# Optimization experiments

Hardware: AMD Instinct MI355X
Metric: run time of the kernel (lower is better)

The kernel has to match this reference:

```python
import itertools
import jax, jax.numpy as jnp
import numpy as np

H, W, DIM, NH, WS = 64, 64, 384, 12, 7
HD = DIM // NH            # head dim = key_dim (attn_ratio=1)
N = WS * WS               # tokens per window
SCALE = HD ** -0.5
EPS = 1e-5
BATCH = 4
HID = int(DIM * 4.0)


def _bias_idxs():
    points = list(itertools.product(range(WS), range(WS)))
    offsets, idxs = {}, []
    for p1 in points:
        for p2 in points:
            off = (abs(p1[0] - p2[0]), abs(p1[1] - p2[1]))
            if off not in offsets:
                offsets[off] = len(offsets)
            idxs.append(offsets[off])
    return np.asarray(idxs, dtype=np.int32).reshape(N, N)

BIAS_IDXS = _bias_idxs()              # [N, N] static
NUM_OFFSETS = int(BIAS_IDXS.max()) + 1  # 49 for a 7x7 window


def setup_inputs() -> dict:
    key = jax.random.key(0)
    ks = jax.random.split(key, 10)
    rn = lambda k, shp, s=0.02: jax.random.normal(k, shp, jnp.float32) * s
    return {
        "x": jax.random.normal(ks[0], (BATCH, H * W, DIM), jnp.float32),
        "ln1_g": jnp.ones((DIM,), jnp.float32),
        "ln1_b": jnp.zeros((DIM,), jnp.float32),
        "qkv_w": rn(ks[1], (DIM, 3 * DIM)),
        "qkv_b": jnp.zeros((3 * DIM,), jnp.float32),
        "proj_w": rn(ks[2], (DIM, DIM)),
        "proj_b": jnp.zeros((DIM,), jnp.float32),
        "attn_bias": rn(ks[3], (NH, NUM_OFFSETS), 0.1),
        "conv_w": rn(ks[4], (DIM, 1, 3, 3), 0.1),  # depthwise OIHW
        "bn_g": jnp.ones((DIM,), jnp.float32),
        "bn_b": jnp.zeros((DIM,), jnp.float32),
        "bn_mean": rn(ks[5], (DIM,), 0.05),
        "bn_var": jax.random.uniform(ks[6], (DIM,), jnp.float32, 0.5, 1.5),
        "ln2_g": jnp.ones((DIM,), jnp.float32),
        "ln2_b": jnp.zeros((DIM,), jnp.float32),
        "fc1_w": rn(ks[7], (DIM, HID)),
        "fc1_b": jnp.zeros((HID,), jnp.float32),
        "fc2_w": rn(ks[8], (HID, DIM)),
        "fc2_b": jnp.zeros((DIM,), jnp.float32),
    }


def _ln(x, g, b):
    m = x.mean(-1, keepdims=True)
    v = jnp.var(x, axis=-1, keepdims=True)
    return (x - m) * jax.lax.rsqrt(v + EPS) * g + b


def reference(x, ln1_g, ln1_b, qkv_w, qkv_b, proj_w, proj_b, attn_bias,
              conv_w, bn_g, bn_b, bn_mean, bn_var, ln2_g, ln2_b,
              fc1_w, fc1_b, fc2_w, fc2_b):
    b, hw, c = x.shape
    res = x
    # --- window partition with padding ---
    pad_b = (-H) % WS
    pad_r = (-W) % WS
    pH, pW = H + pad_b, W + pad_r
    nH, nW = pH // WS, pW // WS
    xw = x.reshape(b, H, W, c)
    xw = jnp.pad(xw, ((0, 0), (0, pad_b), (0, pad_r), (0, 0)))
    xw = xw.reshape(b, nH, WS, nW, WS, c).transpose(0, 1, 3, 2, 4, 5)
    xw = xw.reshape(b * nH * nW, N, c)  # [Bw, N, C]
    # --- attention (pre-LN, relative position bias) ---
    xn = _ln(xw, ln1_g, ln1_b)
    qkv = (xn @ qkv_w + qkv_b).reshape(-1, N, NH, 3 * HD)
    q, k, v = jnp.split(qkv, [HD, 2 * HD], axis=-1)  # each [Bw, N, NH, HD]
    bias = attn_bias[:, BIAS_IDXS]                    # [NH, N, N]
    scores = jnp.einsum('bnhd,bmhd->bhnm', q, k) * SCALE + bias
    a = jax.nn.softmax(scores, axis=-1)
    o = jnp.einsum('bhnm,bmhd->bnhd', a, v).reshape(-1, N, NH * HD)
    xw = o @ proj_w + proj_b
    # --- window reverse + unpad ---
    xw = xw.reshape(b, nH, nW, WS, WS, c).transpose(0, 1, 3, 2, 4, 5)
    xw = xw.reshape(b, pH, pW, c)[:, :H, :W].reshape(b, hw, c)
    x = res + xw
    # --- depthwise 3x3 conv + BatchNorm (eval) ---
    xc = x.transpose(0, 2, 1).reshape(b, c, H, W)
    xc = jax.lax.conv_general_dilated(
        xc, conv_w, (1, 1), ((1, 1), (1, 1)),
        feature_group_count=c,
        dimension_numbers=('NCHW', 'OIHW', 'NCHW'))
    xc = (xc - bn_mean[:, None, None]) * jax.lax.rsqrt(bn_var[:, None, None] + EPS) \
         * bn_g[:, None, None] + bn_b[:, None, None]
    x = xc.reshape(b, c, hw).transpose(0, 2, 1)
    # --- MLP (pre-LN, GELU) with residual ---
    h1 = jax.nn.gelu(_ln(x, ln2_g, ln2_b) @ fc1_w + fc1_b, approximate=False)
    return x + (h1 @ fc2_w + fc2_b)
```

## Files before the change

### kernel.cpp

```cpp
#include <hip/hip_runtime.h>
#include <cstdint>


typedef __bf16 bf16x8 __attribute__((ext_vector_type(8)));
typedef __bf16 bf16x4 __attribute__((ext_vector_type(4)));
typedef float  f32x4  __attribute__((ext_vector_type(4)));

#define DIM_    384
#define QKVD    1152
#define HIDD    1536
#define NTOK    49
#define NWIN    400
#define TOKENS  16384
#define PADROW  16384
#define MQKV    16512
#define SCALE_  0.17677669529663689f
#define EPS_    1e-5f

#define B_LN1   8192
#define B_PADR  1
#define B_TQKV  108
#define B_TPROJ 36
#define B_TFC1  144
#define B_TFC2  144
#define B_CONV  14
#define B_BIAS  192
#define B_TOTAL (B_LN1 + B_PADR + B_TQKV + B_TPROJ + B_TFC1 + B_TFC2 + B_CONV + B_BIAS)

__device__ __forceinline__ void gload_lds16(const void* g, void* l) {
  __builtin_amdgcn_global_load_lds(
      (__attribute__((address_space(1))) void*)g,
      (__attribute__((address_space(3))) void*)l, 16, 0, 0);
}

__device__ __forceinline__ float gelu_fast(float v) {
  float t2 = v * (1.5957691216057308f + 0.07135481627f * v * v);
  return v * __builtin_amdgcn_rcpf(1.f + __expf(-t2));
}

__device__ __forceinline__ void tile_transpose(
    const float* __restrict__ src, __bf16* __restrict__ dst,
    int K, int N, int tile, int tilesN, __bf16 (*ld)[65]) {
  int kt = tile / tilesN, nt = tile % tilesN;
  int k0 = kt * 64, n0 = nt * 64;
  int tid = threadIdx.x;
  int a = tid & 63, b4 = tid >> 6;
  #pragma unroll
  for (int i = 0; i < 16; i++) {
    int kl = b4 + i * 4;
    ld[kl][a] = (__bf16)src[(long)(k0 + kl) * N + n0 + a];
  }
  __syncthreads();
  #pragma unroll
  for (int i = 0; i < 16; i++) {
    int nl = b4 + i * 4;
    dst[(long)(n0 + nl) * K + k0 + a] = ld[a][nl];
  }
}

__global__ __launch_bounds__(256) void prep_all(
    const float* __restrict__ x, const float* __restrict__ ln1_g,
    const float* __restrict__ ln1_b, __bf16* __restrict__ xn,
    const float* __restrict__ qkv_w,  __bf16* __restrict__ wqkv,
    const float* __restrict__ proj_w, __bf16* __restrict__ wproj,
    const float* __restrict__ fc1_w,  __bf16* __restrict__ wfc1,
    const float* __restrict__ fc2_w,  __bf16* __restrict__ wfc2,
    const float* __restrict__ conv_w, float* __restrict__ wconv,
    const float* __restrict__ attn_b, float* __restrict__ bm) {
  __shared__ __bf16 tlds[64][65];
  __shared__ float red[2][4];
  int b = blockIdx.x;
  int tid = threadIdx.x;

  if (b < B_LN1) {
    int sub = tid >> 7, tl = tid & 127;
    long t = (long)b * 2 + sub;
    const float* xr = x + t * DIM_;
    float v0 = xr[tl], v1 = xr[tl + 128], v2 = xr[tl + 256];
    float s = v0 + v1 + v2, s2 = v0 * v0 + v1 * v1 + v2 * v2;
    for (int off = 32; off; off >>= 1) { s += __shfl_down(s, off); s2 += __shfl_down(s2, off); }
    if ((tl & 63) == 0) { red[sub][tl >> 6] = s; red[sub][2 + (tl >> 6)] = s2; }
    __syncthreads();
    float S = red[sub][0] + red[sub][1], S2 = red[sub][2] + red[sub][3];
    float m  = S * (1.f / DIM_);
    float rs = rsqrtf(S2 * (1.f / DIM_) - m * m + EPS_);
    __bf16* orow = xn + t * DIM_;
    orow[tl]       = (__bf16)((v0 - m) * rs * ln1_g[tl]       + ln1_b[tl]);
    orow[tl + 128] = (__bf16)((v1 - m) * rs * ln1_g[tl + 128] + ln1_b[tl + 128]);
    orow[tl + 256] = (__bf16)((v2 - m) * rs * ln1_g[tl + 256] + ln1_b[tl + 256]);
    return;
  }
  b -= B_LN1;
  if (b < B_PADR) {
    for (int i = tid; i < DIM_; i += 256)
      xn[(long)PADROW * DIM_ + i] = (__bf16)ln1_b[i];
    return;
  }
  b -= B_PADR;
  if (b < B_TQKV)  { tile_transpose(qkv_w,  wqkv,  DIM_, QKVD, b, 18, tlds); return; }
  b -= B_TQKV;
  if (b < B_TPROJ) { tile_transpose(proj_w, wproj, DIM_, DIM_, b, 6,  tlds); return; }
  b -= B_TPROJ;
  if (b < B_TFC1)  { tile_transpose(fc1_w,  wfc1,  DIM_, HIDD, b, 24, tlds); return; }
  b -= B_TFC1;
  if (b < B_TFC2)  { tile_transpose(fc2_w,  wfc2,  HIDD, DIM_, b, 6,  tlds); return; }
  b -= B_TFC2;
  if (b < B_CONV) {
    int id = b * 256 + tid;
    if (id < 3456) {
      int ch = id / 9, k = id % 9;
      wconv[k * DIM_ + ch] = conv_w[id];
    }
    return;
  }
  b -= B_CONV;
  {
    int id = b * 256 + tid;
    int h = id >> 12, q = (id >> 6) & 63, kk = id & 63;
    float v;
    if (kk >= NTOK)      v = -1e30f;
    else if (q >= NTOK)  v = 0.f;
    else {
      int idx = abs(q / 7 - kk / 7) * 7 + abs(q % 7 - kk % 7);
      v = attn_b[h * NTOK + idx];
    }
    bm[id] = v;
  }
}

__global__ __launch_bounds__(384) void conv_bn_ln2(
    const float* __restrict__ x1, const float* __restrict__ wT,
    const float* __restrict__ bng, const float* __restrict__ bnb,
    const float* __restrict__ mean, const float* __restrict__ var,
    const float* __restrict__ g2, const float* __restrict__ b2,
    float* __restrict__ x2, __bf16* __restrict__ xln2) {
  int tid = threadIdx.x;
  int p = tid / 96, g = tid % 96;
  int pix = blockIdx.x * 4 + p;
  int bb = pix >> 12, rc = pix & 4095;
  int r = rc >> 6, c = rc & 63;
  int ch = g << 2;

  f32x4 acc = (f32x4){0.f, 0.f, 0.f, 0.f};
  #pragma unroll
  for (int dr = -1; dr <= 1; dr++) {
    int rr = r + dr;
    if (rr < 0 || rr >= 64) continue;
    #pragma unroll
    for (int dc = -1; dc <= 1; dc++) {
      int cc = c + dc;
      if (cc < 0 || cc >= 64) continue;
      f32x4 xv = *(const f32x4*)(x1 + ((long)bb * 4096 + rr * 64 + cc) * DIM_ + ch);
      f32x4 wv = *(const f32x4*)(wT + ((dr + 1) * 3 + (dc + 1)) * DIM_ + ch);
      acc += xv * wv;
    }
  }

  f32x4 gv = *(const f32x4*)(bng + ch);
  f32x4 vv = *(const f32x4*)(var + ch);
  f32x4 mv = *(const f32x4*)(mean + ch);
  f32x4 bv = *(const f32x4*)(bnb + ch);
  f32x4 y;
  #pragma unroll
  for (int j = 0; j < 4; j++) {
    float sc = gv[j] * rsqrtf(vv[j] + EPS_);
    y[j] = acc[j] * sc + (bv[j] - mv[j] * sc);
  }
  *(f32x4*)(x2 + (long)pix * DIM_ + ch) = y;

  __shared__ float pS[4][96], pS2[4][96], mS[4], rS[4];
  pS[p][g]  = y[0] + y[1] + y[2] + y[3];
  pS2[p][g] = y[0] * y[0] + y[1] * y[1] + y[2] * y[2] + y[3] * y[3];
  __syncthreads();
  if (g < 32) {
    float a  = pS[p][g]  + pS[p][g + 32]  + pS[p][g + 64];
    float a2 = pS2[p][g] + pS2[p][g + 32] + pS2[p][g + 64];
    #pragma unroll
    for (int off = 1; off < 32; off <<= 1) {
      a  += __shfl_xor(a, off);
      a2 += __shfl_xor(a2, off);
    }
    if (g == 0) {
      float m = a * (1.f / DIM_);
      mS[p] = m;
      rS[p] = rsqrtf(a2 * (1.f / DIM_) - m * m + EPS_);
    }
  }
  __syncthreads();
  float m = mS[p], rs = rS[p];
  f32x4 gg = *(const f32x4*)(g2 + ch);
  f32x4 b2v = *(const f32x4*)(b2 + ch);
  bf16x4 ov;
  #pragma unroll
  for (int j = 0; j < 4; j++) ov[j] = (__bf16)((y[j] - m) * rs * gg[j] + b2v[j]);
  *(bf16x4*)(xln2 + (long)pix * DIM_ + ch) = ov;
}

__global__ __launch_bounds__(64) void attn_mfma(const __bf16* __restrict__ qkv,
                                                const float* __restrict__ bm,
                                                __bf16* __restrict__ o) {
  int blk = blockIdx.x;
  int win = blk / 12, h = blk % 12;
  int bb = win / 100, rem = win % 100;
  int wy = rem / 10, wx = rem % 10;
  int lane = threadIdx.x;
  int quad = lane >> 4, l16 = lane & 15;

  __shared__ __align__(16) __bf16 Vt[32][72];
  __shared__ __align__(16) __bf16 P[64][72];

  const __bf16* base = qkv + h * 96;

  bf16x8 qf[4], kf[4];
  #pragma unroll
  for (int mt = 0; mt < 4; mt++) {
    int t = mt * 16 + l16;
    int ty = t / 7, tx = t % 7;
    int r = wy * 7 + ty, c = wx * 7 + tx;
    int row = (t < NTOK && r < 64 && c < 64) ? (bb * 4096 + r * 64 + c) : PADROW;
    const __bf16* rp = base + (long)row * QKVD + quad * 8;
    qf[mt] = *(const bf16x8*)(rp);
    kf[mt] = *(const bf16x8*)(rp + 32);
  }
  {
    int t = lane;
    int ty = t / 7, tx = t % 7;
    int r = wy * 7 + ty, c = wx * 7 + tx;
    int row = (t < NTOK && r < 64 && c < 64) ? (bb * 4096 + r * 64 + c) : PADROW;
    const __bf16* vp = base + (long)row * QKVD + 64;
    bf16x8 vv[4];
    #pragma unroll
    for (int i = 0; i < 4; i++) vv[i] = *(const bf16x8*)(vp + i * 8);
    #pragma unroll
    for (int i = 0; i < 4; i++)
      #pragma unroll
      for (int j = 0; j < 8; j++) Vt[i * 8 + j][lane] = vv[i][j];
  }

  f32x4 S[4][4];
  #pragma unroll
  for (int i = 0; i < 4; i++)
    #pragma unroll
    for (int j = 0; j < 4; j++) S[i][j] = (f32x4){0.f, 0.f, 0.f, 0.f};
  #pragma unroll
  for (int mt = 0; mt < 4; mt++)
    #pragma unroll
    for (int nt = 0; nt < 4; nt++)
      S[mt][nt] = __builtin_amdgcn_mfma_f32_16x16x32_bf16(qf[mt], kf[nt], S[mt][nt], 0, 0, 0);

  const float* bmh = bm + h * 4096;
  #pragma unroll
  for (int mt = 0; mt < 4; mt++)
    #pragma unroll
    for (int r = 0; r < 4; r++) {
      int q = mt * 16 + quad * 4 + r;
      #pragma unroll
      for (int nt = 0; nt < 4; nt++)
        S[mt][nt][r] = S[mt][nt][r] * SCALE_ + bmh[q * 64 + nt * 16 + l16];
    }

  #pragma unroll
  for (int mt = 0; mt < 4; mt++)
    #pragma unroll
    for (int r = 0; r < 4; r++) {
      float mx = fmaxf(fmaxf(S[mt][0][r], S[mt][1][r]), fmaxf(S[mt][2][r], S[mt][3][r]));
      #pragma unroll
      for (int off = 1; off < 16; off <<= 1) mx = fmaxf(mx, __shfl_xor(mx, off));
      float sum = 0.f;
      #pragma unroll
      for (int nt = 0; nt < 4; nt++) {
        float e = __expf(S[mt][nt][r] - mx);
        S[mt][nt][r] = e;
        sum += e;
      }
      #pragma unroll
      for (int off = 1; off < 16; off <<= 1) sum += __shfl_xor(sum, off);
      float inv = 1.f / sum;
      #pragma unroll
      for (int nt = 0; nt < 4; nt++) S[mt][nt][r] *= inv;
    }

  #pragma unroll
  for (int mt = 0; mt < 4; mt++)
    #pragma unroll
    for (int r = 0; r < 4; r++) {
      int q = mt * 16 + quad * 4 + r;
      #pragma unroll
      for (int nt = 0; nt < 4; nt++)
        P[q][nt * 16 + l16] = (__bf16)S[mt][nt][r];
    }
  __syncthreads();

  f32x4 O[4][2];
  #pragma unroll
  for (int i = 0; i < 4; i++)
    #pragma unroll
    for (int j = 0; j < 2; j++) O[i][j] = (f32x4){0.f, 0.f, 0.f, 0.f};
  #pragma unroll
  for (int kt = 0; kt < 2; kt++) {
    bf16x8 pf[4], vf[2];
    #pragma unroll
    for (int mt = 0; mt < 4; mt++)
      pf[mt] = *(const bf16x8*)(&P[mt * 16 + l16][kt * 32 + quad * 8]);
    #pragma unroll
    for (int nt = 0; nt < 2; nt++)
      vf[nt] = *(const bf16x8*)(&Vt[nt * 16 + l16][kt * 32 + quad * 8]);
    #pragma unroll
    for (int mt = 0; mt < 4; mt++)
      #pragma unroll
      for (int nt = 0; nt < 2; nt++)
        O[mt][nt] = __builtin_amdgcn_mfma_f32_16x16x32_bf16(pf[mt], vf[nt], O[mt][nt], 0, 0, 0);
  }

  #pragma unroll
  for (int mt = 0; mt < 4; mt++)
    #pragma unroll
    for (int r = 0; r < 4; r++) {
      int q = mt * 16 + quad * 4 + r;
      if (q < NTOK) {
        int ty = q / 7, tx = q % 7;
        int rr = wy * 7 + ty, cc = wx * 7 + tx;
        if (rr < 64 && cc < 64) {
          __bf16* ob = o + ((long)bb * 4096 + rr * 64 + cc) * DIM_ + h * 32;
          #pragma unroll
          for (int nt = 0; nt < 2; nt++)
            ob[nt * 16 + l16] = (__bf16)O[mt][nt][r];
        }
      }
    }
}

template <int MODE, int TN>
__global__ void __launch_bounds__(256)
gemm_bf16(const __bf16* __restrict__ A, const __bf16* __restrict__ Bt,
          const float* __restrict__ bias, int K, int N,
          float* __restrict__ outf, __bf16* __restrict__ outb,
          const float* __restrict__ res) {
  constexpr int NT = TN / 32;
  __shared__ __align__(16) __bf16 sA[128 * 32];
  int tid = threadIdx.x, lane = tid & 63, wid = tid >> 6;
  int wm = wid >> 1, wn = wid & 1;
  int quad = lane >> 4, l16 = lane & 15;
  long tileM = (long)blockIdx.x * 128;
  long tileN = (long)blockIdx.y * TN;

  f32x4 acc[4][NT];
  #pragma unroll
  for (int i = 0; i < 4; i++)
    #pragma unroll
    for (int j = 0; j < NT; j++) acc[i][j] = (f32x4){0.f, 0.f, 0.f, 0.f};

  int rr = wid * 16 + (lane >> 2);
  const __bf16* gA = A + (tileM + rr) * (long)K + ((lane & 3) << 3);
  const long rowskip = 64 * (long)K;
  const __bf16* bP[NT];
  #pragma unroll
  for (int nt = 0; nt < NT; nt++)
    bP[nt] = Bt + (tileN + wn * (TN / 2) + nt * 16 + l16) * (long)K + (quad << 3);

  for (int k0 = 0; k0 < K; k0 += 32) {
    gload_lds16(gA + k0,           sA + (wid << 9));
    gload_lds16(gA + k0 + rowskip, sA + ((wid + 4) << 9));
    bf16x8 bfr[NT];
    #pragma unroll
    for (int nt = 0; nt < NT; nt++) bfr[nt] = *(const bf16x8*)(bP[nt] + k0);
    __syncthreads();
    bf16x8 af[4];
    #pragma unroll
    for (int mt = 0; mt < 4; mt++)
      af[mt] = *(const bf16x8*)(sA + ((wm * 64 + mt * 16 + l16) << 5) + (quad << 3));
    #pragma unroll
    for (int mt = 0; mt < 4; mt++)
      #pragma unroll
      for (int nt = 0; nt < NT; nt++)
        acc[mt][nt] = __builtin_amdgcn_mfma_f32_16x16x32_bf16(af[mt], bfr[nt], acc[mt][nt], 0, 0, 0);
    __syncthreads();
  }

  float bcol[NT];
  #pragma unroll
  for (int nt = 0; nt < NT; nt++) bcol[nt] = bias[tileN + wn * (TN / 2) + nt * 16 + l16];

  #pragma unroll
  for (int mt = 0; mt < 4; mt++) {
    #pragma unroll
    for (int r = 0; r < 4; r++) {
      long row = tileM + wm * 64 + mt * 16 + quad * 4 + r;
      if (MODE == 0) {
        __bf16* orow = outb + row * (long)N;
        #pragma unroll
        for (int nt = 0; nt < NT; nt++)
          orow[tileN + wn * (TN / 2) + nt * 16 + l16] = (__bf16)(acc[mt][nt][r] + bcol[nt]);
      } else if (MODE == 2) {
        __bf16* orow = outb + row * (long)N;
        #pragma unroll
        for (int nt = 0; nt < NT; nt++) {
          float v = acc[mt][nt][r] + bcol[nt];
          orow[tileN + wn * (TN / 2) + nt * 16 + l16] = (__bf16)gelu_fast(v);
        }
      } else {
        float* orow = outf + row * (long)N;
        const float* rrow = res + row * (long)N;
        #pragma unroll
        for (int nt = 0; nt < NT; nt++) {
          long col = tileN + wn * (TN / 2) + nt * 16 + l16;
          orow[col] = acc[mt][nt][r] + bcol[nt] + rrow[col];
        }
      }
    }
  }
}

extern "C" void kernel_launch(void* const* d_in, const int* in_sizes, int n_in,
                              void* d_out, int out_size, void* d_ws, size_t ws_size,
                              hipStream_t stream) {
  const float* x       = (const float*)d_in[0];
  const float* ln1_g   = (const float*)d_in[1];
  const float* ln1_b   = (const float*)d_in[2];
  const float* qkv_w   = (const float*)d_in[3];
  const float* qkv_b   = (const float*)d_in[4];
  const float* proj_w  = (const float*)d_in[5];
  const float* proj_b  = (const float*)d_in[6];
  const float* attn_b  = (const float*)d_in[7];
  const float* conv_w  = (const float*)d_in[8];
  const float* bn_g    = (const float*)d_in[9];
  const float* bn_b    = (const float*)d_in[10];
  const float* bn_mean = (const float*)d_in[11];
  const float* bn_var  = (const float*)d_in[12];
  const float* ln2_g   = (const float*)d_in[13];
  const float* ln2_b   = (const float*)d_in[14];
  const float* fc1_w   = (const float*)d_in[15];
  const float* fc1_b   = (const float*)d_in[16];
  const float* fc2_w   = (const float*)d_in[17];
  const float* fc2_b   = (const float*)d_in[18];

  char* p = (char*)d_ws;
  __bf16* WQKV = (__bf16*)p;  p += 884736;
  __bf16* WPROJ = (__bf16*)p; p += 294912;
  __bf16* WFC1 = (__bf16*)p;  p += 1179648;
  __bf16* WFC2 = (__bf16*)p;  p += 1179648;
  float*  WCONV = (float*)p;  p += 13824;
  char* region = p;           p += 63307776;
  float* X1 = (float*)p;      p += 25165824;
  float* X2 = (float*)p;      p += 25165824;
  __bf16* XN   = (__bf16*)region;
  __bf16* QKVB = (__bf16*)(region + 12681216);
  __bf16* OBUF = (__bf16*)(region + 50724864);
  __bf16* XLN2 = (__bf16*)region;
  __bf16* H1   = (__bf16*)(region + 12681216);
  float*  BM   = X1;
  float* OUT = (float*)d_out;

  prep_all<<<B_TOTAL, 256, 0, stream>>>(x, ln1_g, ln1_b, XN,
                                        qkv_w, WQKV, proj_w, WPROJ,
                                        fc1_w, WFC1, fc2_w, WFC2,
                                        conv_w, WCONV, attn_b, BM);

  gemm_bf16<0, 128><<<dim3(MQKV / 128, QKVD / 128), 256, 0, stream>>>(
      XN, WQKV, qkv_b, DIM_, QKVD, nullptr, QKVB, nullptr);

  attn_mfma<<<NWIN * 12, 64, 0, stream>>>(QKVB, BM, OBUF);

  gemm_bf16<3, 64><<<dim3(TOKENS / 128, DIM_ / 64), 256, 0, stream>>>(
      OBUF, WPROJ, proj_b, DIM_, DIM_, X1, nullptr, x);

  conv_bn_ln2<<<TOKENS / 4, 384, 0, stream>>>(X1, WCONV, bn_g, bn_b, bn_mean, bn_var,
                                              ln2_g, ln2_b, X2, XLN2);

  gemm_bf16<2, 128><<<dim3(TOKENS / 128, HIDD / 128), 256, 0, stream>>>(
      XLN2, WFC1, fc1_b, DIM_, HIDD, nullptr, H1, nullptr);

  gemm_bf16<3, 64><<<dim3(TOKENS / 128, DIM_ / 64), 256, 0, stream>>>(
      H1, WFC2, fc2_b, HIDD, DIM_, OUT, nullptr, X2);
}
```

Baseline: 322.5 us.

## Stage GEMM B tiles through LDS and add K=64 FC2 kernel

The generic bf16 GEMM now loads the weight (B) tile into shared memory with direct global-to-LDS loads, instead of each wave reading B fragments straight from global memory. A new FC2-specific kernel handles the K=1536 GEMM by loading two 32-wide K slices per iteration, which halves the number of barriers per K step. The aim is to cut redundant global traffic for B and the synchronisation overhead, at the cost of more LDS per block.

New measurement: 278.6 us. 1.16x faster.

```diff
diff --git a/kernel.cpp b/kernel.cpp
--- a/kernel.cpp
+++ b/kernel.cpp
@@ -338,6 +338,7 @@
           const float* __restrict__ res) {
   constexpr int NT = TN / 32;
   __shared__ __align__(16) __bf16 sA[128 * 32];
+  __shared__ __align__(16) __bf16 sB[TN * 32];
   int tid = threadIdx.x, lane = tid & 63, wid = tid >> 6;
   int wm = wid >> 1, wn = wid & 1;
   int quad = lane >> 4, l16 = lane & 15;
@@ -351,24 +352,24 @@
     for (int j = 0; j < NT; j++) acc[i][j] = (f32x4){0.f, 0.f, 0.f, 0.f};
 
   int rr = wid * 16 + (lane >> 2);
-  const __bf16* gA = A + (tileM + rr) * (long)K + ((lane & 3) << 3);
+  const __bf16* gA = A  + (tileM + rr) * (long)K + ((lane & 3) << 3);
+  const __bf16* gB = Bt + (tileN + rr) * (long)K + ((lane & 3) << 3);
   const long rowskip = 64 * (long)K;
-  const __bf16* bP[NT];
-  #pragma unroll
-  for (int nt = 0; nt < NT; nt++)
-    bP[nt] = Bt + (tileN + wn * (TN / 2) + nt * 16 + l16) * (long)K + (quad << 3);
 
   for (int k0 = 0; k0 < K; k0 += 32) {
     gload_lds16(gA + k0,           sA + (wid << 9));
     gload_lds16(gA + k0 + rowskip, sA + ((wid + 4) << 9));
-    bf16x8 bfr[NT];
-    #pragma unroll
-    for (int nt = 0; nt < NT; nt++) bfr[nt] = *(const bf16x8*)(bP[nt] + k0);
+    gload_lds16(gB + k0,           sB + (wid << 9));
+    if (TN == 128)
+      gload_lds16(gB + k0 + rowskip, sB + ((wid + 4) << 9));
     __syncthreads();
-    bf16x8 af[4];
+    bf16x8 af[4], bfr[NT];
     #pragma unroll
     for (int mt = 0; mt < 4; mt++)
       af[mt] = *(const bf16x8*)(sA + ((wm * 64 + mt * 16 + l16) << 5) + (quad << 3));
+    #pragma unroll
+    for (int nt = 0; nt < NT; nt++)
+      bfr[nt] = *(const bf16x8*)(sB + ((wn * (TN / 2) + nt * 16 + l16) << 5) + (quad << 3));
     #pragma unroll
     for (int mt = 0; mt < 4; mt++)
       #pragma unroll
@@ -411,6 +412,77 @@
   }
 }
 
+__global__ void __launch_bounds__(256)
+gemm_fc2_k64(const __bf16* __restrict__ A, const __bf16* __restrict__ Bt,
+             const float* __restrict__ bias, int K, int N,
+             float* __restrict__ outf, const float* __restrict__ res) {
+  constexpr int TN = 64, NT = 2;
+  __shared__ __align__(16) __bf16 sA[2][128 * 32];
+  __shared__ __align__(16) __bf16 sB[2][TN * 32];
+  int tid = threadIdx.x, lane = tid & 63, wid = tid >> 6;
+  int wm = wid >> 1, wn = wid & 1;
+  int quad = lane >> 4, l16 = lane & 15;
+  long tileM = (long)blockIdx.x * 128;
+  long tileN = (long)blockIdx.y * TN;
+
+  f32x4 acc[4][NT];
+  #pragma unroll
+  for (int i = 0; i < 4; i++)
+    #pragma unroll
+    for (int j = 0; j < NT; j++) acc[i][j] = (f32x4){0.f, 0.f, 0.f, 0.f};
+
+  int rr = wid * 16 + (lane >> 2);
+  const __bf16* gA = A  + (tileM + rr) * (long)K + ((lane & 3) << 3);
+  const __bf16* gB = Bt + (tileN + rr) * (long)K + ((lane & 3) << 3);
+  const long rowskip = 64 * (long)K;
+
+  for (int k0 = 0; k0 < K; k0 += 64) {
+    #pragma unroll
+    for (int h = 0; h < 2; h++) {
+      const int ko = k0 + h * 32;
+      gload_lds16(gA + ko,           &sA[h][wid << 9]);
+      gload_lds16(gA + ko + rowskip, &sA[h][(wid + 4) << 9]);
+      gload_lds16(gB + ko,           &sB[h][wid << 9]);
+    }
+    __syncthreads();
+    #pragma unroll
+    for (int h = 0; h < 2; h++) {
+      bf16x8 af[4], bfr[NT];
+      #pragma unroll
+      for (int mt = 0; mt < 4; mt++)
+        af[mt] = *(const bf16x8*)(&sA[h][((wm * 64 + mt * 16 + l16) << 5) + (quad << 3)]);
+      #pragma unroll
+      for (int nt = 0; nt < NT; nt++)
+        bfr[nt] = *(const bf16x8*)(&sB[h][((wn * 32 + nt * 16 + l16) << 5) + (quad << 3)]);
+      #pragma unroll
+      for (int mt = 0; mt < 4; mt++)
+        #pragma unroll
+        for (int nt = 0; nt < NT; nt++)
+          acc[mt][nt] = __builtin_amdgcn_mfma_f32_16x16x32_bf16(af[mt], bfr[nt], acc[mt][nt], 0, 0, 0);
+    }
+    __syncthreads();
+  }
+
+  float bcol[NT];
+  #pragma unroll
+  for (int nt = 0; nt < NT; nt++) bcol[nt] = bias[tileN + wn * 32 + nt * 16 + l16];
+
+  #pragma unroll
+  for (int mt = 0; mt < 4; mt++) {
+    #pragma unroll
+    for (int r = 0; r < 4; r++) {
+      long row = tileM + wm * 64 + mt * 16 + quad * 4 + r;
+      float* orow = outf + row * (long)N;
+      const float* rrow = res + row * (long)N;
+      #pragma unroll
+      for (int nt = 0; nt < NT; nt++) {
+        long col = tileN + wn * 32 + nt * 16 + l16;
+        orow[col] = acc[mt][nt][r] + bcol[nt] + rrow[col];
+      }
+    }
+  }
+}
+
 extern "C" void kernel_launch(void* const* d_in, const int* in_sizes, int n_in,
                               void* d_out, int out_size, void* d_ws, size_t ws_size,
                               hipStream_t stream) {
@@ -470,6 +542,6 @@
   gemm_bf16<2, 128><<<dim3(TOKENS / 128, HIDD / 128), 256, 0, stream>>>(
       XLN2, WFC1, fc1_b, DIM_, HIDD, nullptr, H1, nullptr);
 
-  gemm_bf16<3, 64><<<dim3(TOKENS / 128, DIM_ / 64), 256, 0, stream>>>(
-      H1, WFC2, fc2_b, HIDD, DIM_, OUT, nullptr, X2);
-}
+  gemm_fc2_k64<<<dim3(TOKENS / 128, DIM_ / 64), 256, 0, stream>>>(
+      H1, WFC2, fc2_b, HIDD, DIM_, OUT, X2);
+}
```

## Stage B tiles in LDS with K=64 steps and store intermediates as bf16

Applied to the files above, without the earlier changes.

Replaces the GEMM with a variant that stages both the A and B tiles into LDS using swizzled slots. Each barrier pair now covers two 32-wide K halves, and all GEMMs use a fixed 64-wide N tile. The intermediate residual buffers X1 and X2 are stored as bf16 instead of fp32, and the attention bias mask gets its own buffer. The aim is to cut global memory traffic and barrier count, and to drop uncoalesced direct B loads from global memory. The risk is precision loss on the residual path and more blocks for the QKV and FC1 GEMMs, which reload the A tiles more often.

New measurement: 283.9 us. 1.14x faster.

```diff
diff --git a/kernel.cpp b/kernel.cpp
--- a/kernel.cpp
+++ b/kernel.cpp
@@ -129,11 +129,11 @@
 }
 
 __global__ __launch_bounds__(384) void conv_bn_ln2(
-    const float* __restrict__ x1, const float* __restrict__ wT,
+    const __bf16* __restrict__ x1, const float* __restrict__ wT,
     const float* __restrict__ bng, const float* __restrict__ bnb,
     const float* __restrict__ mean, const float* __restrict__ var,
     const float* __restrict__ g2, const float* __restrict__ b2,
-    float* __restrict__ x2, __bf16* __restrict__ xln2) {
+    __bf16* __restrict__ x2, __bf16* __restrict__ xln2) {
   int tid = threadIdx.x;
   int p = tid / 96, g = tid % 96;
   int pix = blockIdx.x * 4 + p;
@@ -150,9 +150,10 @@
     for (int dc = -1; dc <= 1; dc++) {
       int cc = c + dc;
       if (cc < 0 || cc >= 64) continue;
-      f32x4 xv = *(const f32x4*)(x1 + ((long)bb * 4096 + rr * 64 + cc) * DIM_ + ch);
+      bf16x4 xb = *(const bf16x4*)(x1 + ((long)bb * 4096 + rr * 64 + cc) * DIM_ + ch);
       f32x4 wv = *(const f32x4*)(wT + ((dr + 1) * 3 + (dc + 1)) * DIM_ + ch);
-      acc += xv * wv;
+      #pragma unroll
+      for (int j = 0; j < 4; j++) acc[j] += (float)xb[j] * wv[j];
     }
   }
 
@@ -166,7 +167,12 @@
     float sc = gv[j] * rsqrtf(vv[j] + EPS_);
     y[j] = acc[j] * sc + (bv[j] - mv[j] * sc);
   }
-  *(f32x4*)(x2 + (long)pix * DIM_ + ch) = y;
+  {
+    bf16x4 xv2;
+    #pragma unroll
+    for (int j = 0; j < 4; j++) xv2[j] = (__bf16)y[j];
+    *(bf16x4*)(x2 + (long)pix * DIM_ + ch) = xv2;
+  }
 
   __shared__ float pS[4][96], pS2[4][96], mS[4], rS[4];
   pS[p][g]  = y[0] + y[1] + y[2] + y[3];
@@ -330,14 +336,15 @@
     }
 }
 
-template <int MODE, int TN>
+template <int MODE>
 __global__ void __launch_bounds__(256)
-gemm_bf16(const __bf16* __restrict__ A, const __bf16* __restrict__ Bt,
-          const float* __restrict__ bias, int K, int N,
-          float* __restrict__ outf, __bf16* __restrict__ outb,
-          const float* __restrict__ res) {
-  constexpr int NT = TN / 32;
-  __shared__ __align__(16) __bf16 sA[128 * 32];
+gemm_k64(const __bf16* __restrict__ A, const __bf16* __restrict__ Bt,
+         const float* __restrict__ bias, int K, int N,
+         float* __restrict__ outf, __bf16* __restrict__ outb,
+         const void* __restrict__ res) {
+  constexpr int TN = 64, NT = 2;
+  __shared__ __align__(16) __bf16 sA[2][128 * 32];
+  __shared__ __align__(16) __bf16 sB[2][TN * 32];
   int tid = threadIdx.x, lane = tid & 63, wid = tid >> 6;
   int wm = wid >> 1, wn = wid & 1;
   int quad = lane >> 4, l16 = lane & 15;
@@ -351,35 +358,42 @@
     for (int j = 0; j < NT; j++) acc[i][j] = (f32x4){0.f, 0.f, 0.f, 0.f};
 
   int rr = wid * 16 + (lane >> 2);
-  const __bf16* gA = A + (tileM + rr) * (long)K + ((lane & 3) << 3);
+  int sc = ((lane & 3) - (lane >> 3)) & 3;
+  const __bf16* gA = A  + (tileM + rr) * (long)K + (sc << 3);
+  const __bf16* gB = Bt + (tileN + rr) * (long)K + (sc << 3);
   const long rowskip = 64 * (long)K;
-  const __bf16* bP[NT];
-  #pragma unroll
-  for (int nt = 0; nt < NT; nt++)
-    bP[nt] = Bt + (tileN + wn * (TN / 2) + nt * 16 + l16) * (long)K + (quad << 3);
-
-  for (int k0 = 0; k0 < K; k0 += 32) {
-    gload_lds16(gA + k0,           sA + (wid << 9));
-    gload_lds16(gA + k0 + rowskip, sA + ((wid + 4) << 9));
-    bf16x8 bfr[NT];
-    #pragma unroll
-    for (int nt = 0; nt < NT; nt++) bfr[nt] = *(const bf16x8*)(bP[nt] + k0);
+  int slot = (((l16 >> 1) + quad) & 3) << 3;
+
+  for (int k0 = 0; k0 < K; k0 += 64) {
+    #pragma unroll
+    for (int h = 0; h < 2; h++) {
+      const int ko = k0 + h * 32;
+      gload_lds16(gA + ko,           &sA[h][wid << 9]);
+      gload_lds16(gA + ko + rowskip, &sA[h][(wid + 4) << 9]);
+      gload_lds16(gB + ko,           &sB[h][wid << 9]);
+    }
     __syncthreads();
-    bf16x8 af[4];
-    #pragma unroll
-    for (int mt = 0; mt < 4; mt++)
-      af[mt] = *(const bf16x8*)(sA + ((wm * 64 + mt * 16 + l16) << 5) + (quad << 3));
-    #pragma unroll
-    for (int mt = 0; mt < 4; mt++)
+    #pragma unroll
+    for (int h = 0; h < 2; h++) {
+      bf16x8 af[4], bfr[NT];
+      #pragma unroll
+      for (int mt = 0; mt < 4; mt++)
+        af[mt] = *(const bf16x8*)(&sA[h][((wm * 64 + mt * 16 + l16) << 5) + slot]);
       #pragma unroll
       for (int nt = 0; nt < NT; nt++)
-        acc[mt][nt] = __builtin_amdgcn_mfma_f32_16x16x32_bf16(af[mt], bfr[nt], acc[mt][nt], 0, 0, 0);
+        bfr[nt] = *(const bf16x8*)(&sB[h][((wn * 32 + nt * 16 + l16) << 5) + slot]);
+      #pragma unroll
+      for (int mt = 0; mt < 4; mt++)
+        #pragma unroll
+        for (int nt = 0; nt < NT; nt++)
+          acc[mt][nt] = __builtin_amdgcn_mfma_f32_16x16x32_bf16(af[mt], bfr[nt], acc[mt][nt], 0, 0, 0);
+    }
     __syncthreads();
   }
 
   float bcol[NT];
   #pragma unroll
-  for (int nt = 0; nt < NT; nt++) bcol[nt] = bias[tileN + wn * (TN / 2) + nt * 16 + l16];
+  for (int nt = 0; nt < NT; nt++) bcol[nt] = bias[tileN + wn * 32 + nt * 16 + l16];
 
   #pragma unroll
   for (int mt = 0; mt < 4; mt++) {
@@ -390,21 +404,29 @@
         __bf16* orow = outb + row * (long)N;
         #pragma unroll
         for (int nt = 0; nt < NT; nt++)
-          orow[tileN + wn * (TN / 2) + nt * 16 + l16] = (__bf16)(acc[mt][nt][r] + bcol[nt]);
+          orow[tileN + wn * 32 + nt * 16 + l16] = (__bf16)(acc[mt][nt][r] + bcol[nt]);
       } else if (MODE == 2) {
         __bf16* orow = outb + row * (long)N;
         #pragma unroll
         for (int nt = 0; nt < NT; nt++) {
           float v = acc[mt][nt][r] + bcol[nt];
-          orow[tileN + wn * (TN / 2) + nt * 16 + l16] = (__bf16)gelu_fast(v);
+          orow[tileN + wn * 32 + nt * 16 + l16] = (__bf16)gelu_fast(v);
+        }
+      } else if (MODE == 4) {
+        float* orow = outf + row * (long)N;
+        const __bf16* rrow = (const __bf16*)res + row * (long)N;
+        #pragma unroll
+        for (int nt = 0; nt < NT; nt++) {
+          long col = tileN + wn * 32 + nt * 16 + l16;
+          orow[col] = acc[mt][nt][r] + bcol[nt] + (float)rrow[col];
         }
       } else {
-        float* orow = outf + row * (long)N;
-        const float* rrow = res + row * (long)N;
+        __bf16* orow = outb + row * (long)N;
+        const float* rrow = (const float*)res + row * (long)N;
         #pragma unroll
         for (int nt = 0; nt < NT; nt++) {
-          long col = tileN + wn * (TN / 2) + nt * 16 + l16;
-          orow[col] = acc[mt][nt][r] + bcol[nt] + rrow[col];
+          long col = tileN + wn * 32 + nt * 16 + l16;
+          orow[col] = (__bf16)(acc[mt][nt][r] + bcol[nt] + rrow[col]);
         }
       }
     }
@@ -441,14 +463,15 @@
   __bf16* WFC2 = (__bf16*)p;  p += 1179648;
   float*  WCONV = (float*)p;  p += 13824;
   char* region = p;           p += 63307776;
-  float* X1 = (float*)p;      p += 25165824;
-  float* X2 = (float*)p;      p += 25165824;
+  float* BMbuf = (float*)p;   p += 196608;
+  __bf16* X1 = (__bf16*)p;    p += 12582912;
+  __bf16* X2 = (__bf16*)p;    p += 12582912;
   __bf16* XN   = (__bf16*)region;
   __bf16* QKVB = (__bf16*)(region + 12681216);
   __bf16* OBUF = (__bf16*)(region + 50724864);
   __bf16* XLN2 = (__bf16*)region;
   __bf16* H1   = (__bf16*)(region + 12681216);
-  float*  BM   = X1;
+  float*  BM   = BMbuf;
   float* OUT = (float*)d_out;
 
   prep_all<<<B_TOTAL, 256, 0, stream>>>(x, ln1_g, ln1_b, XN,
@@ -456,20 +479,20 @@
                                         fc1_w, WFC1, fc2_w, WFC2,
                                         conv_w, WCONV, attn_b, BM);
 
-  gemm_bf16<0, 128><<<dim3(MQKV / 128, QKVD / 128), 256, 0, stream>>>(
+  gemm_k64<0><<<dim3(MQKV / 128, QKVD / 64), 256, 0, stream>>>(
       XN, WQKV, qkv_b, DIM_, QKVD, nullptr, QKVB, nullptr);
 
   attn_mfma<<<NWIN * 12, 64, 0, stream>>>(QKVB, BM, OBUF);
 
-  gemm_bf16<3, 64><<<dim3(TOKENS / 128, DIM_ / 64), 256, 0, stream>>>(
-      OBUF, WPROJ, proj_b, DIM_, DIM_, X1, nullptr, x);
+  gemm_k64<5><<<dim3(TOKENS / 128, DIM_ / 64), 256, 0, stream>>>(
+      OBUF, WPROJ, proj_b, DIM_, DIM_, nullptr, X1, x);
 
   conv_bn_ln2<<<TOKENS / 4, 384, 0, stream>>>(X1, WCONV, bn_g, bn_b, bn_mean, bn_var,
                                               ln2_g, ln2_b, X2, XLN2);
 
-  gemm_bf16<2, 128><<<dim3(TOKENS / 128, HIDD / 128), 256, 0, stream>>>(
+  gemm_k64<2><<<dim3(TOKENS / 128, HIDD / 64), 256, 0, stream>>>(
       XLN2, WFC1, fc1_b, DIM_, HIDD, nullptr, H1, nullptr);
 
-  gemm_bf16<3, 64><<<dim3(TOKENS / 128, DIM_ / 64), 256, 0, stream>>>(
+  gemm_k64<4><<<dim3(TOKENS / 128, DIM_ / 64), 256, 0, stream>>>(
       H1, WFC2, fc2_b, HIDD, DIM_, OUT, nullptr, X2);
 }
```
